# Optimization experiments

Hardware: AMD Instinct MI355X
Metric: run time of the kernel (lower is better)

## Reference

```python
import jax, jax.numpy as jnp
import numpy as np

N, M, D = 6144, 6144, 128
EPS = 1e-12


def setup_inputs() -> dict:
    key = jax.random.key(0)
    k1, k2 = jax.random.split(key)
    desc1 = jax.random.normal(k1, (N, D), dtype=jnp.float32)
    desc2 = jax.random.normal(k2, (M, D), dtype=jnp.float32)
    # DISK descriptors are unit-normalized; distances in the docstring are in [0, 2]
    desc1 = desc1 / jnp.linalg.norm(desc1, axis=-1, keepdims=True)
    desc2 = desc2 / jnp.linalg.norm(desc2, axis=-1, keepdims=True)
    inverse_T = jnp.asarray(15.0, dtype=jnp.float32)  # learned scalar nn.Parameter
    return {"desc1": desc1, "desc2": desc2, "inverse_T": inverse_T}


def reference(desc1, desc2, inverse_T):
    # pairwise Euclidean distance matrix [N, M]
    sq1 = jnp.sum(desc1 * desc1, axis=-1)            # [N]
    sq2 = jnp.sum(desc2 * desc2, axis=-1)            # [M]
    inner = desc1 @ desc2.T                           # [N, M] GEMM, D=128
    d2 = sq1[:, None] + sq2[None, :] - 2.0 * inner
    distances = jnp.sqrt(jnp.maximum(d2, 0.0) + EPS)  # [N, M]

    affinity = -inverse_T * distances                 # scaled logits

    # Categorical(logits=affinity).logits  == log_softmax over rows
    # Categorical(logits=affinity.T).logits.T == log_softmax over columns
    logp_I = jax.nn.log_softmax(affinity, axis=1)     # row distribution [N, M]
    logp_T = jax.nn.log_softmax(affinity, axis=0)     # col distribution [N, M]

    dense_logp = logp_I + logp_T                      # dual-softmax log prob
    dense_p = jnp.exp(logp_I) * jnp.exp(logp_T)       # dual-softmax prob

    # mle(): argmax matches with cycle-consistency check
    maxes_I = jnp.argmax(affinity, axis=1)            # [N] best col per row
    maxes_T = jnp.argmax(affinity, axis=0)            # [M] best row per col
    idx = jnp.arange(N)
    cycle_consistent = maxes_T[maxes_I] == idx        # [N] bool mask
    # Original returns stack([right[paired_left], paired_left]) over the
    # consistent subset; here we keep fixed shape [2, N] + the mask
    # (matches[:, i] valid iff cycle_consistent[i]).
    matches = jnp.stack([idx, maxes_I], axis=0)       # [2, N] int

    return dense_logp, dense_p, matches, cycle_consistent
```

## Files before the change

kernel.cpp:

```cpp
#include <hip/hip_runtime.h>
#include <hip/hip_bf16.h>
#include <stdint.h>

#define NROWS 6144
#define MCOLS 6144
#define DDIM  128
#define EPSQ  1e-12f
#define NTC   48

typedef unsigned long long ull;
typedef __attribute__((ext_vector_type(8))) short short8;
typedef __attribute__((ext_vector_type(4))) float floatx4;

__device__ __forceinline__ ull makeKey(float v, int idx) {
    unsigned u = __float_as_uint(v);
    u = (u & 0x80000000u) ? ~u : (u | 0x80000000u);
    return ((ull)u << 32) | (ull)(0xFFFFFFFFu - (unsigned)idx);
}
__device__ __forceinline__ int decodeKeyIdx(ull k) {
    return (int)(0xFFFFFFFFu - (unsigned)(k & 0xFFFFFFFFull));
}
__device__ __forceinline__ unsigned short f2bf(float f) {
    unsigned u = __float_as_uint(f);
    u += 0x7fffu + ((u >> 16) & 1);
    return (unsigned short)(u >> 16);
}

#define DPPF(x, ctrl) __uint_as_float(__builtin_amdgcn_update_dpp( \
    0, (int)__float_as_uint(x), (ctrl), 0xF, 0xF, false))
#define DPPI(x, ctrl) __builtin_amdgcn_update_dpp(0, (x), (ctrl), 0xF, 0xF, false)
#define ROR8 0x128
#define ROR4 0x124
#define ROR2 0x122
#define ROR1 0x121

#define GLOAD16(g, l) \
  __builtin_amdgcn_global_load_lds((const __attribute__((address_space(1))) unsigned int*)(g), \
                                   (__attribute__((address_space(3))) unsigned int*)(l), 16, 0, 0)

__device__ __forceinline__ void tileCoord(int& rowBase, int& colBase) {
    int id  = blockIdx.x;
    int wid = (id & 7) * (NTC * NTC / 8) + (id >> 3);
    rowBase = (wid / NTC) * 128;
    colBase = (wid % NTC) * 128;
}

__global__ __launch_bounds__(256) void convert_kernel(
    const float* __restrict__ d1, const float* __restrict__ d2,
    unsigned short* __restrict__ s1, unsigned short* __restrict__ s2,
    float* __restrict__ sq1, float* __restrict__ sq2,
    unsigned* __restrict__ zero_region)
{
    int tid = blockIdx.x * 256 + threadIdx.x;
    if (tid < 36864) zero_region[tid] = 0u;

    int row = tid >> 4;
    int sub = tid & 15;
    if (row >= NROWS + MCOLS) return;
    bool isA = row < NROWS;
    int r = isA ? row : row - NROWS;
    const float* src = (isA ? d1 : d2) + (size_t)r * DDIM + sub * 8;
    unsigned short* dst = (isA ? s1 : s2) + (size_t)r * 256;

    float4 v0 = *(const float4*)(src);
    float4 v1 = *(const float4*)(src + 4);
    float vs[8] = {v0.x, v0.y, v0.z, v0.w, v1.x, v1.y, v1.z, v1.w};

    float s = 0.f;
    #pragma unroll
    for (int j = 0; j < 8; ++j) s += vs[j] * vs[j];
    #pragma unroll
    for (int m = 1; m < 16; m <<= 1) s += __shfl_xor(s, m, 64);
    if (sub == 0) { if (isA) sq1[r] = s; else sq2[r] = s; }

    short8 hi, lo;
    #pragma unroll
    for (int j = 0; j < 8; ++j) {
        unsigned short h = f2bf(vs[j]);
        hi[j] = (short)h;
        lo[j] = (short)f2bf(vs[j] - __uint_as_float((unsigned)h << 16));
    }
    int e  = sub * 8;
    int c  = e >> 6;
    int pe = (e & 63) ^ ((r & 7) << 3);
    *(short8*)(dst + c * 128 + pe)      = hi;
    *(short8*)(dst + c * 128 + 64 + pe) = lo;
}

__device__ __forceinline__ void stageBuf(
    const unsigned short* __restrict__ gpanel, unsigned short* buf,
    int c, int h, int t)
{
    #pragma unroll
    for (int it = 0; it < 2; ++it) {
        int li = t * 8 + it * 4096;
        int r  = li >> 6, e = li & 63;
        int gi = r * 256 + c * 128 + h * 64 + e;
        GLOAD16(gpanel + gi, &buf[li]);
    }
}

__device__ __forceinline__ void computeChunk2(
    const unsigned short* Ah_, const unsigned short* Al_,
    const unsigned short* Bh_,
    int lane, int wr, int wc, floatx4 acc[4][2])
{
    const int l15 = lane & 15;
    const int q16 = (lane >> 4) * 16;
    const int sw  = (l15 & 7) << 4;
    const char* Ah = (const char*)Ah_;
    const char* Al = (const char*)Al_;
    const char* Bh = (const char*)Bh_;
    #pragma unroll
    for (int ks = 0; ks < 2; ++ks) {
        const int kk = (ks * 64 + q16) ^ sw;
        short8 afh[4], afl[4], bfh[2];
        #pragma unroll
        for (int mi = 0; mi < 4; ++mi) {
            afh[mi] = *(const short8*)(Ah + (wr * 64 + mi * 16 + l15) * 128 + kk);
            afl[mi] = *(const short8*)(Al + (wr * 64 + mi * 16 + l15) * 128 + kk);
        }
        #pragma unroll
        for (int ni = 0; ni < 2; ++ni)
            bfh[ni] = *(const short8*)(Bh + (wc * 32 + ni * 16 + l15) * 128 + kk);
        #pragma unroll
        for (int mi = 0; mi < 4; ++mi)
            #pragma unroll
            for (int ni = 0; ni < 2; ++ni)
                acc[mi][ni] = __builtin_amdgcn_mfma_f32_16x16x32_bf16(
                    bfh[ni], afh[mi], acc[mi][ni], 0, 0, 0);
        #pragma unroll
        for (int mi = 0; mi < 4; ++mi)
            #pragma unroll
            for (int ni = 0; ni < 2; ++ni)
                acc[mi][ni] = __builtin_amdgcn_mfma_f32_16x16x32_bf16(
                    bfh[ni], afl[mi], acc[mi][ni], 0, 0, 0);
    }
}

__global__ __launch_bounds__(512, 4) void gemm_reduce_kernel(
    const unsigned short* __restrict__ s1, const unsigned short* __restrict__ s2,
    const float* __restrict__ invT,
    const float* __restrict__ sq1, const float* __restrict__ sq2,
    float* __restrict__ rowsum, float* __restrict__ colsum,
    ull* __restrict__ rowkey, ull* __restrict__ colkey)
{
    __shared__ float lRowS[128], lColS[128];
    __shared__ ull   lRowK[128], lColK[128];

    const int t = threadIdx.x;
    const int lane = t & 63;
    const int wave = t >> 6;
    const int wr = wave >> 2, wc = wave & 3;
    int rowBase, colBase;
    tileCoord(rowBase, colBase);
    const char* gA = (const char*)(s1 + (size_t)rowBase * 256);
    const char* gB = (const char*)(s2 + (size_t)colBase * 256);

    if (t < 128) { lRowS[t] = 0.f; lColS[t] = 0.f; lRowK[t] = 0ull; lColK[t] = 0ull; }

    const int l15 = lane & 15;
    const int q16 = (lane >> 4) * 16;
    const int sw  = (l15 & 7) << 4;
    int aOff[4], bOff[2];
    #pragma unroll
    for (int mi = 0; mi < 4; ++mi) aOff[mi] = (wr * 64 + mi * 16 + l15) * 512;
    #pragma unroll
    for (int ni = 0; ni < 2; ++ni) bOff[ni] = (wc * 32 + ni * 16 + l15) * 512;

    floatx4 acc[4][2] = {};
    #pragma unroll
    for (int c = 0; c < 2; ++c) {
        #pragma unroll
        for (int ks = 0; ks < 2; ++ks) {
            const int kb = c * 256 + ((ks * 64 + q16) ^ sw);
            short8 afh[4], afl[4], bfh[2], bfl[2];
            #pragma unroll
            for (int mi = 0; mi < 4; ++mi) {
                afh[mi] = *(const short8*)(gA + aOff[mi] + kb);
                afl[mi] = *(const short8*)(gA + aOff[mi] + kb + 128);
            }
            #pragma unroll
            for (int ni = 0; ni < 2; ++ni) {
                bfh[ni] = *(const short8*)(gB + bOff[ni] + kb);
                bfl[ni] = *(const short8*)(gB + bOff[ni] + kb + 128);
            }
            #pragma unroll
            for (int mi = 0; mi < 4; ++mi)
                #pragma unroll
                for (int ni = 0; ni < 2; ++ni)
                    acc[mi][ni] = __builtin_amdgcn_mfma_f32_16x16x32_bf16(
                        bfh[ni], afh[mi], acc[mi][ni], 0, 0, 0);
            #pragma unroll
            for (int mi = 0; mi < 4; ++mi)
                #pragma unroll
                for (int ni = 0; ni < 2; ++ni)
                    acc[mi][ni] = __builtin_amdgcn_mfma_f32_16x16x32_bf16(
                        bfl[ni], afh[mi], acc[mi][ni], 0, 0, 0);
            #pragma unroll
            for (int mi = 0; mi < 4; ++mi)
                #pragma unroll
                for (int ni = 0; ni < 2; ++ni)
                    acc[mi][ni] = __builtin_amdgcn_mfma_f32_16x16x32_bf16(
                        bfh[ni], afl[mi], acc[mi][ni], 0, 0, 0);
        }
    }

    const int q = lane >> 4;
    const float iT = *invT;
    float s1r[4];
    #pragma unroll
    for (int mi = 0; mi < 4; ++mi)
        s1r[mi] = sq1[rowBase + wr * 64 + mi * 16 + l15] + EPSQ;
    const int colLoc0 = wc * 32 + q * 4;
    float4 s2v[2];
    #pragma unroll
    for (int ni = 0; ni < 2; ++ni)
        s2v[ni] = *(const float4*)(sq2 + colBase + colLoc0 + ni * 16);

    float rs[4], rv[4]; int rj[4];
    float cs[2][4], cv[2][4]; int ci[2][4];
    #pragma unroll
    for (int ni = 0; ni < 2; ++ni)
        #pragma unroll
        for (int r = 0; r < 4; ++r) { cs[ni][r] = 0.f; cv[ni][r] = -1e30f; ci[ni][r] = 0; }

    #pragma unroll
    for (int mi = 0; mi < 4; ++mi) {
        const int gi = rowBase + wr * 64 + mi * 16 + l15;
        rs[mi] = 0.f; rv[mi] = -1e30f; rj[mi] = 0;
        #pragma unroll
        for (int ni = 0; ni < 2; ++ni) {
            #pragma unroll
            for (int r = 0; r < 4; ++r) {
                float sv2 = (r == 0) ? s2v[ni].x : (r == 1) ? s2v[ni].y
                          : (r == 2) ? s2v[ni].z : s2v[ni].w;
                float dd = s1r[mi] + sv2 - 2.0f * acc[mi][ni][r];
                float v = -iT * __builtin_amdgcn_sqrtf(fmaxf(dd, EPSQ));
                float e = __expf(v);
                rs[mi] += e;
                if (v > rv[mi]) { rv[mi] = v; rj[mi] = colBase + colLoc0 + ni * 16 + r; }
                cs[ni][r] += e;
                if (v > cv[ni][r]) { cv[ni][r] = v; ci[ni][r] = gi; }
            }
        }
    }

    __syncthreads();

    #pragma unroll
    for (int mi = 0; mi < 4; ++mi) {
        float s = rs[mi];
        s += __shfl_xor(s, 16, 64); s += __shfl_xor(s, 32, 64);
        float v = rv[mi];
        v = fmaxf(v, __shfl_xor(v, 16, 64)); v = fmaxf(v, __shfl_xor(v, 32, 64));
        int cand = (rv[mi] == v) ? rj[mi] : 0x7FFFFFFF;
        cand = min(cand, __shfl_xor(cand, 16, 64));
        cand = min(cand, __shfl_xor(cand, 32, 64));
        if (lane < 16) {
            int idx = wr * 64 + mi * 16 + l15;
            atomicAdd(&lRowS[idx], s);
            atomicMax(&lRowK[idx], makeKey(v, cand));
        }
    }

    #pragma unroll
    for (int ni = 0; ni < 2; ++ni)
        #pragma unroll
        for (int r = 0; r < 4; ++r) {
            float s = cs[ni][r];
            s += DPPF(s, ROR8); s += DPPF(s, ROR4); s += DPPF(s, ROR2); s += DPPF(s, ROR1);
            float v = cv[ni][r];
            v = fmaxf(v, DPPF(v, ROR8)); v = fmaxf(v, DPPF(v, ROR4));
            v = fmaxf(v, DPPF(v, ROR2)); v = fmaxf(v, DPPF(v, ROR1));
            int cand = (cv[ni][r] == v) ? ci[ni][r] : 0x7FFFFFFF;
            cand = min(cand, DPPI(cand, ROR8)); cand = min(cand, DPPI(cand, ROR4));
            cand = min(cand, DPPI(cand, ROR2)); cand = min(cand, DPPI(cand, ROR1));
            if (l15 == 0) {
                int idx = colLoc0 + ni * 16 + r;
                atomicAdd(&lColS[idx], s);
                atomicMax(&lColK[idx], makeKey(v, cand));
            }
        }
    __syncthreads();

    if (t < 128) {
        atomicAdd(&rowsum[rowBase + t], lRowS[t]);
        atomicMax(&rowkey[rowBase + t], lRowK[t]);
    } else if (t < 256) {
        int j = t - 128;
        atomicAdd(&colsum[colBase + j], lColS[j]);
        atomicMax(&colkey[colBase + j], lColK[j]);
    }
}

#define VSTRIDE 132
__global__ __launch_bounds__(512, 4) void gemm_write_kernel(
    const unsigned short* __restrict__ s1, const unsigned short* __restrict__ s2,
    const float* __restrict__ invT,
    const float* __restrict__ sq1, const float* __restrict__ sq2,
    const float* __restrict__ rowsum, const float* __restrict__ colsum,
    const ull* __restrict__ rowkey, const ull* __restrict__ colkey,
    float* __restrict__ logp_out, float* __restrict__ p_out,
    float* __restrict__ out_matches, float* __restrict__ out_cyc)
{
    __shared__ char SMEM[128 * VSTRIDE * 4];
    unsigned short* A0 = (unsigned short*)(SMEM);
    unsigned short* A1 = (unsigned short*)(SMEM + 16384);
    unsigned short* B0 = (unsigned short*)(SMEM + 32768);
    unsigned short* B1 = (unsigned short*)(SMEM + 49152);
    float* V = (float*)SMEM;

    const int t = threadIdx.x;
    const int lane = t & 63;
    const int wave = t >> 6;
    const int wr = wave >> 2, wc = wave & 3;
    int rowBase, colBase;
    tileCoord(rowBase, colBase);
    const unsigned short* gA = s1 + (size_t)rowBase * 256;
    const unsigned short* gB = s2 + (size_t)colBase * 256;

    if (colBase == 0 && t < 128) {
        int i = rowBase + t;
        int mi = decodeKeyIdx(rowkey[i]);
        out_matches[i]         = (float)i;
        out_matches[NROWS + i] = (float)mi;
        out_cyc[i] = (decodeKeyIdx(colkey[mi]) == i) ? 1.0f : 0.0f;
    }

    floatx4 acc[4][2] = {};
    stageBuf(gA, A0, 0, 0, t); stageBuf(gA, A1, 0, 1, t);
    stageBuf(gB, B0, 0, 0, t); stageBuf(gB, B1, 1, 0, t);
    __syncthreads();
    computeChunk2(A0, A1, B0, lane, wr, wc, acc);
    __syncthreads();
    stageBuf(gA, A0, 1, 0, t); stageBuf(gA, A1, 1, 1, t);
    __syncthreads();
    computeChunk2(A0, A1, B1, lane, wr, wc, acc);

    const int l15 = lane & 15;
    const int q   = lane >> 4;
    const float iT = *invT;
    float s1r[4];
    #pragma unroll
    for (int mi = 0; mi < 4; ++mi)
        s1r[mi] = sq1[rowBase + wr * 64 + mi * 16 + l15] + EPSQ;
    const int colLoc0 = wc * 32 + q * 4;
    float4 s2v[2];
    #pragma unroll
    for (int ni = 0; ni < 2; ++ni)
        s2v[ni] = *(const float4*)(sq2 + colBase + colLoc0 + ni * 16);

    __syncthreads();
    #pragma unroll
    for (int mi = 0; mi < 4; ++mi) {
        const int lrow = wr * 64 + mi * 16 + l15;
        #pragma unroll
        for (int ni = 0; ni < 2; ++ni) {
            floatx4 vv;
            #pragma unroll
            for (int r = 0; r < 4; ++r) {
                float sv2 = (r == 0) ? s2v[ni].x : (r == 1) ? s2v[ni].y
                          : (r == 2) ? s2v[ni].z : s2v[ni].w;
                float dd = s1r[mi] + sv2 - 2.0f * acc[mi][ni][r];
                vv[r] = -iT * __builtin_amdgcn_sqrtf(fmaxf(dd, EPSQ));
            }
            *(floatx4*)(V + lrow * VSTRIDE + colLoc0 + ni * 16) = vv;
        }
    }
    __syncthreads();

    const int rsub = lane >> 4;
    const int csub = (lane & 15) * 4;
    #pragma unroll
    for (int g = 0; g < 4; ++g) {
        const int lrow = wave * 16 + g * 4 + rsub;
        const int grow = rowBase + lrow;
        const float rl = logf(rowsum[grow]);
        #pragma unroll
        for (int h = 0; h < 2; ++h) {
            const int lcol = h * 64 + csub;
            float4 csum = *(const float4*)(colsum + colBase + lcol);
            float4 cl;
            cl.x = logf(csum.x); cl.y = logf(csum.y);
            cl.z = logf(csum.z); cl.w = logf(csum.w);
            float4 v4 = *(const float4*)(V + lrow * VSTRIDE + lcol);
            floatx4 ov, pv;
            ov[0] = (v4.x - rl) + (v4.x - cl.x); pv[0] = __expf(ov[0]);
            ov[1] = (v4.y - rl) + (v4.y - cl.y); pv[1] = __expf(ov[1]);
            ov[2] = (v4.z - rl) + (v4.z - cl.z); pv[2] = __expf(ov[2]);
            ov[3] = (v4.w - rl) + (v4.w - cl.w); pv[3] = __expf(ov[3]);
            size_t off = (size_t)grow * MCOLS + colBase + lcol;
            __builtin_nontemporal_store(ov, (floatx4*)(logp_out + off));
            __builtin_nontemporal_store(pv, (floatx4*)(p_out + off));
        }
    }
}

extern "C" void kernel_launch(void* const* d_in, const int* in_sizes, int n_in,
                              void* d_out, int out_size, void* d_ws, size_t ws_size,
                              hipStream_t stream) {
    const float* d1   = (const float*)d_in[0];
    const float* d2   = (const float*)d_in[1];
    const float* invT = (const float*)d_in[2];

    float* out     = (float*)d_out;
    float* logp    = out;
    float* pout    = out + (size_t)NROWS * MCOLS;
    float* matches = out + 2ull * NROWS * MCOLS;
    float* cyc     = matches + 2 * NROWS;

    char* ws = (char*)d_ws;
    float* rowsum = (float*)(ws + 0);
    float* colsum = (float*)(ws + 24576);
    ull*   rowkey = (ull*)(ws + 49152);
    ull*   colkey = (ull*)(ws + 98304);
    float* sq1    = (float*)(ws + 147456);
    float* sq2    = (float*)(ws + 172032);
    unsigned short* s1 = (unsigned short*)(ws + 270336);
    unsigned short* s2 = (unsigned short*)(ws + 270336 + 3145728);

    convert_kernel<<<(NROWS + MCOLS) * 16 / 256, 256, 0, stream>>>(
        d1, d2, s1, s2, sq1, sq2, (unsigned*)ws);

    gemm_reduce_kernel<<<NTC * NTC, 512, 0, stream>>>(
        s1, s2, invT, sq1, sq2, rowsum, colsum, rowkey, colkey);

    gemm_write_kernel<<<NTC * NTC, 512, 0, stream>>>(
        s1, s2, invT, sq1, sq2, rowsum, colsum, rowkey, colkey,
        logp, pout, matches, cyc);
}
```

Measured before the change: 135.1 us.

## Stage split-bf16 GEMM operands through LDS in reduce kernel

The reduce kernel used to load MFMA fragments straight from global memory. It now stages A and B hi/lo panels into three 16KB LDS buffers in a fixed, barrier-separated sequence and reuses them across the three split-precision products. The launch bound rises to 6 waves-per-SIMD occupancy, and one redundant barrier is dropped. This adds LDS use and several syncthreads with no double buffering, and the higher occupancy target may cause register pressure or spills.

```diff
diff --git a/kernel.cpp b/kernel.cpp
--- a/kernel.cpp
+++ b/kernel.cpp
@@ -100,51 +100,79 @@
     }
 }
 
-__device__ __forceinline__ void computeChunk2(
-    const unsigned short* Ah_, const unsigned short* Al_,
-    const unsigned short* Bh_,
+__device__ __forceinline__ void computeSplit(
+    const unsigned short* Ab_, const unsigned short* Bb_,
     int lane, int wr, int wc, floatx4 acc[4][2])
 {
     const int l15 = lane & 15;
     const int q16 = (lane >> 4) * 16;
     const int sw  = (l15 & 7) << 4;
-    const char* Ah = (const char*)Ah_;
-    const char* Al = (const char*)Al_;
-    const char* Bh = (const char*)Bh_;
+    const char* Ab = (const char*)Ab_;
+    const char* Bb = (const char*)Bb_;
     #pragma unroll
     for (int ks = 0; ks < 2; ++ks) {
         const int kk = (ks * 64 + q16) ^ sw;
-        short8 afh[4], afl[4], bfh[2];
-        #pragma unroll
-        for (int mi = 0; mi < 4; ++mi) {
-            afh[mi] = *(const short8*)(Ah + (wr * 64 + mi * 16 + l15) * 128 + kk);
-            afl[mi] = *(const short8*)(Al + (wr * 64 + mi * 16 + l15) * 128 + kk);
-        }
+        short8 af[4], bf[2];
+        #pragma unroll
+        for (int mi = 0; mi < 4; ++mi)
+            af[mi] = *(const short8*)(Ab + (wr * 64 + mi * 16 + l15) * 128 + kk);
         #pragma unroll
         for (int ni = 0; ni < 2; ++ni)
-            bfh[ni] = *(const short8*)(Bh + (wc * 32 + ni * 16 + l15) * 128 + kk);
+            bf[ni] = *(const short8*)(Bb + (wc * 32 + ni * 16 + l15) * 128 + kk);
         #pragma unroll
         for (int mi = 0; mi < 4; ++mi)
             #pragma unroll
             for (int ni = 0; ni < 2; ++ni)
                 acc[mi][ni] = __builtin_amdgcn_mfma_f32_16x16x32_bf16(
-                    bfh[ni], afh[mi], acc[mi][ni], 0, 0, 0);
+                    bf[ni], af[mi], acc[mi][ni], 0, 0, 0);
+    }
+}
+
+__device__ __forceinline__ void computeSplitAB2(
+    const unsigned short* Ab_, const unsigned short* B0_, const unsigned short* B1_,
+    int lane, int wr, int wc, floatx4 acc[4][2])
+{
+    const int l15 = lane & 15;
+    const int q16 = (lane >> 4) * 16;
+    const int sw  = (l15 & 7) << 4;
+    const char* Ab = (const char*)Ab_;
+    const char* B0 = (const char*)B0_;
+    const char* B1 = (const char*)B1_;
+    #pragma unroll
+    for (int ks = 0; ks < 2; ++ks) {
+        const int kk = (ks * 64 + q16) ^ sw;
+        short8 af[4], bf0[2], bf1[2];
+        #pragma unroll
+        for (int mi = 0; mi < 4; ++mi)
+            af[mi] = *(const short8*)(Ab + (wr * 64 + mi * 16 + l15) * 128 + kk);
+        #pragma unroll
+        for (int ni = 0; ni < 2; ++ni) {
+            bf0[ni] = *(const short8*)(B0 + (wc * 32 + ni * 16 + l15) * 128 + kk);
+            bf1[ni] = *(const short8*)(B1 + (wc * 32 + ni * 16 + l15) * 128 + kk);
+        }
         #pragma unroll
         for (int mi = 0; mi < 4; ++mi)
             #pragma unroll
             for (int ni = 0; ni < 2; ++ni)
                 acc[mi][ni] = __builtin_amdgcn_mfma_f32_16x16x32_bf16(
-                    bfh[ni], afl[mi], acc[mi][ni], 0, 0, 0);
-    }
-}
-
-__global__ __launch_bounds__(512, 4) void gemm_reduce_kernel(
+                    bf0[ni], af[mi], acc[mi][ni], 0, 0, 0);
+        #pragma unroll
+        for (int mi = 0; mi < 4; ++mi)
+            #pragma unroll
+            for (int ni = 0; ni < 2; ++ni)
+                acc[mi][ni] = __builtin_amdgcn_mfma_f32_16x16x32_bf16(
+                    bf1[ni], af[mi], acc[mi][ni], 0, 0, 0);
+    }
+}
+
+__global__ __launch_bounds__(512, 6) void gemm_reduce_kernel(
     const unsigned short* __restrict__ s1, const unsigned short* __restrict__ s2,
     const float* __restrict__ invT,
     const float* __restrict__ sq1, const float* __restrict__ sq2,
     float* __restrict__ rowsum, float* __restrict__ colsum,
     ull* __restrict__ rowkey, ull* __restrict__ colkey)
 {
+    __shared__ unsigned short P[8192], Q[8192], R[8192];
     __shared__ float lRowS[128], lColS[128];
     __shared__ ull   lRowK[128], lColK[128];
 
@@ -154,59 +182,30 @@
     const int wr = wave >> 2, wc = wave & 3;
     int rowBase, colBase;
     tileCoord(rowBase, colBase);
-    const char* gA = (const char*)(s1 + (size_t)rowBase * 256);
-    const char* gB = (const char*)(s2 + (size_t)colBase * 256);
+    const unsigned short* gA = s1 + (size_t)rowBase * 256;
+    const unsigned short* gB = s2 + (size_t)colBase * 256;
 
     if (t < 128) { lRowS[t] = 0.f; lColS[t] = 0.f; lRowK[t] = 0ull; lColK[t] = 0ull; }
 
+    floatx4 acc[4][2] = {};
+    stageBuf(gA, P, 0, 0, t); stageBuf(gB, Q, 0, 0, t); stageBuf(gB, R, 0, 1, t);
+    __syncthreads();
+    computeSplitAB2(P, Q, R, lane, wr, wc, acc);
+    __syncthreads();
+    stageBuf(gA, R, 0, 1, t); stageBuf(gA, P, 1, 0, t);
+    __syncthreads();
+    computeSplit(R, Q, lane, wr, wc, acc);
+    __syncthreads();
+    stageBuf(gB, Q, 1, 0, t); stageBuf(gB, R, 1, 1, t);
+    __syncthreads();
+    computeSplitAB2(P, Q, R, lane, wr, wc, acc);
+    __syncthreads();
+    stageBuf(gA, R, 1, 1, t);
+    __syncthreads();
+    computeSplit(R, Q, lane, wr, wc, acc);
+
     const int l15 = lane & 15;
-    const int q16 = (lane >> 4) * 16;
-    const int sw  = (l15 & 7) << 4;
-    int aOff[4], bOff[2];
-    #pragma unroll
-    for (int mi = 0; mi < 4; ++mi) aOff[mi] = (wr * 64 + mi * 16 + l15) * 512;
-    #pragma unroll
-    for (int ni = 0; ni < 2; ++ni) bOff[ni] = (wc * 32 + ni * 16 + l15) * 512;
-
-    floatx4 acc[4][2] = {};
-    #pragma unroll
-    for (int c = 0; c < 2; ++c) {
-        #pragma unroll
-        for (int ks = 0; ks < 2; ++ks) {
-            const int kb = c * 256 + ((ks * 64 + q16) ^ sw);
-            short8 afh[4], afl[4], bfh[2], bfl[2];
-            #pragma unroll
-            for (int mi = 0; mi < 4; ++mi) {
-                afh[mi] = *(const short8*)(gA + aOff[mi] + kb);
-                afl[mi] = *(const short8*)(gA + aOff[mi] + kb + 128);
-            }
-            #pragma unroll
-            for (int ni = 0; ni < 2; ++ni) {
-                bfh[ni] = *(const short8*)(gB + bOff[ni] + kb);
-                bfl[ni] = *(const short8*)(gB + bOff[ni] + kb + 128);
-            }
-            #pragma unroll
-            for (int mi = 0; mi < 4; ++mi)
-                #pragma unroll
-                for (int ni = 0; ni < 2; ++ni)
-                    acc[mi][ni] = __builtin_amdgcn_mfma_f32_16x16x32_bf16(
-                        bfh[ni], afh[mi], acc[mi][ni], 0, 0, 0);
-            #pragma unroll
-            for (int mi = 0; mi < 4; ++mi)
-                #pragma unroll
-                for (int ni = 0; ni < 2; ++ni)
-                    acc[mi][ni] = __builtin_amdgcn_mfma_f32_16x16x32_bf16(
-                        bfl[ni], afh[mi], acc[mi][ni], 0, 0, 0);
-            #pragma unroll
-            for (int mi = 0; mi < 4; ++mi)
-                #pragma unroll
-                for (int ni = 0; ni < 2; ++ni)
-                    acc[mi][ni] = __builtin_amdgcn_mfma_f32_16x16x32_bf16(
-                        bfh[ni], afl[mi], acc[mi][ni], 0, 0, 0);
-        }
-    }
-
-    const int q = lane >> 4;
+    const int q   = lane >> 4;
     const float iT = *invT;
     float s1r[4];
     #pragma unroll
@@ -245,8 +244,6 @@
             }
         }
     }
-
-    __syncthreads();
 
     #pragma unroll
     for (int mi = 0; mi < 4; ++mi) {
@@ -291,6 +288,44 @@
         int j = t - 128;
         atomicAdd(&colsum[colBase + j], lColS[j]);
         atomicMax(&colkey[colBase + j], lColK[j]);
+    }
+}
+
+__device__ __forceinline__ void computeChunk2(
+    const unsigned short* Ah_, const unsigned short* Al_,
+    const unsigned short* Bh_,
+    int lane, int wr, int wc, floatx4 acc[4][2])
+{
+    const int l15 = lane & 15;
+    const int q16 = (lane >> 4) * 16;
+    const int sw  = (l15 & 7) << 4;
+    const char* Ah = (const char*)Ah_;
+    const char* Al = (const char*)Al_;
+    const char* Bh = (const char*)Bh_;
+    #pragma unroll
+    for (int ks = 0; ks < 2; ++ks) {
+        const int kk = (ks * 64 + q16) ^ sw;
+        short8 afh[4], afl[4], bfh[2];
+        #pragma unroll
+        for (int mi = 0; mi < 4; ++mi) {
+            afh[mi] = *(const short8*)(Ah + (wr * 64 + mi * 16 + l15) * 128 + kk);
+            afl[mi] = *(const short8*)(Al + (wr * 64 + mi * 16 + l15) * 128 + kk);
+        }
+        #pragma unroll
+        for (int ni = 0; ni < 2; ++ni)
+            bfh[ni] = *(const short8*)(Bh + (wc * 32 + ni * 16 + l15) * 128 + kk);
+        #pragma unroll
+        for (int mi = 0; mi < 4; ++mi)
+            #pragma unroll
+            for (int ni = 0; ni < 2; ++ni)
+                acc[mi][ni] = __builtin_amdgcn_mfma_f32_16x16x32_bf16(
+                    bfh[ni], afh[mi], acc[mi][ni], 0, 0, 0);
+        #pragma unroll
+        for (int mi = 0; mi < 4; ++mi)
+            #pragma unroll
+            for (int ni = 0; ni < 2; ++ni)
+                acc[mi][ni] = __builtin_amdgcn_mfma_f32_16x16x32_bf16(
+                    bfh[ni], afl[mi], acc[mi][ni], 0, 0, 0);
     }
 }
 
```

Result: slower. 138.5 us (+2.5%).
